# Kernel tuning notes

Measured on AMD Instinct MI355X. Metric: run time of the kernel, lower is better.

The kernel has to match this reference:

```python
import jax, jax.numpy as jnp
import numpy as np

NUM_HEADS = 8
EPS = 1e-6


def setup_inputs() -> dict:
    key = jax.random.key(0)
    k1, k2, k3 = jax.random.split(key, 3)
    B, N, C = 4, 256, 512
    x = jax.random.normal(k1, (B, N, C), dtype=jnp.float32)
    w_qkv = jax.random.normal(k2, (3 * C, C), dtype=jnp.float32) * (C ** -0.5)
    w_proj = jax.random.normal(k3, (C, C), dtype=jnp.float32) * (C ** -0.5)
    b_proj = jnp.zeros((C,), dtype=jnp.float32)
    paramR = jnp.ones((1,), dtype=jnp.float32)
    return {"x": x, "w_qkv": w_qkv, "w_proj": w_proj, "b_proj": b_proj, "paramR": paramR}


def _fourier_attention(x, w_qkv, w_proj, b_proj, paramR):
    B, N, C = x.shape
    H = NUM_HEADS
    Dh = C // H
    # qkv projection (no bias), split into per-head q,k,v: (B,H,N,Dh)
    qkv = jnp.einsum('bnc,kc->bnk', x, w_qkv).reshape(B, N, 3, H, Dh)
    q = qkv[:, :, 0].transpose(0, 2, 1, 3)
    k = qkv[:, :, 1].transpose(0, 2, 1, 3)
    v = qkv[:, :, 2].transpose(0, 2, 1, 3)
    R = paramR[0]
    # Generalized Fourier integral kernel: prod_d sin(R*(q_d - k_d))/(q_d - k_d)
    diff = q[:, :, :, None, :] - k[:, :, None, :, :]  # (B,H,Nq,Nk,Dh)
    near0 = jnp.abs(diff) < 1e-8
    safe = jnp.where(near0, jnp.float32(1.0), diff)
    s = jnp.where(near0, R, jnp.sin(R * safe) / safe)
    score = jnp.prod(s, axis=-1)  # (B,H,Nq,Nk)
    a4 = score ** 4
    attn = a4 / (jnp.sum(a4, axis=-1, keepdims=True) + EPS)  # normalize over keys
    out = jnp.einsum('bhqk,bhkd->bhqd', attn, v)
    out = out.transpose(0, 2, 1, 3).reshape(B, N, C)
    return jnp.einsum('bnc,oc->bno', out, w_proj) + b_proj


def reference(x, w_qkv, w_proj, b_proj, paramR):
    return _fourier_attention(x, w_qkv, w_proj, b_proj, paramR)
```

## Files before the change

kernel.cpp:

```cpp
#include <hip/hip_runtime.h>
#include <math.h>

#define BB 4
#define NN 256
#define CC 512
#define HH 8
#define DH 64

typedef __attribute__((ext_vector_type(8))) short bf16x8;
typedef __attribute__((ext_vector_type(4))) float f32x4;

__device__ inline unsigned short f2bf(float f) {
  unsigned u = __float_as_uint(f);
  u += 0x7FFFu + ((u >> 16) & 1u);
  return (unsigned short)(u >> 16);
}
__device__ inline float bf2f(unsigned short s) {
  return __uint_as_float((unsigned)s << 16);
}

__global__ __launch_bounds__(256) void cvt_hilo(
    const float* __restrict__ in, unsigned short* __restrict__ h,
    unsigned short* __restrict__ l, int n) {
  int i = (blockIdx.x * 256 + threadIdx.x) * 4;
  if (i >= n) return;
  float4 f = *(const float4*)(in + i);
  float fa[4] = {f.x, f.y, f.z, f.w};
  ushort4 hv, lv;
  unsigned short* hp = (unsigned short*)&hv;
  unsigned short* lp = (unsigned short*)&lv;
#pragma unroll
  for (int j = 0; j < 4; j++) {
    unsigned short hb = f2bf(fa[j]);
    hp[j] = hb;
    lp[j] = f2bf(fa[j] - bf2f(hb));
  }
  *(ushort4*)(h + i) = hv;
  *(ushort4*)(l + i) = lv;
}

template <bool BIAS>
__global__ __launch_bounds__(256, 2) void gemm_mfma(
    const unsigned short* __restrict__ Ah, const unsigned short* __restrict__ Al,
    const unsigned short* __restrict__ Bh, const unsigned short* __restrict__ Bl,
    const float* __restrict__ bias, float* __restrict__ C, int M, int N,
    int K) {
  __shared__ unsigned short sAh[128][40], sAl[128][40];
  __shared__ unsigned short sBh[128][40], sBl[128][40];
  const int t = threadIdx.x;
  const int lane = t & 63;
  const int w = t >> 6;
  const int bm = blockIdx.y * 128;
  const int bn = blockIdx.x * 128;
  const int wr = (w >> 1) * 64;
  const int wc = (w & 1) * 64;
  const int quad = lane >> 4;
  const int l16 = lane & 15;

  f32x4 acc[4][4];
#pragma unroll
  for (int i = 0; i < 4; i++)
#pragma unroll
    for (int j = 0; j < 4; j++) {
      acc[i][j][0] = 0.f;
      acc[i][j][1] = 0.f;
      acc[i][j][2] = 0.f;
      acc[i][j][3] = 0.f;
    }

  for (int k0 = 0; k0 < K; k0 += 32) {
    __syncthreads();
#pragma unroll
    for (int s = 0; s < 2; s++) {
      int slot = t + 256 * s;
      int r = slot >> 2;
      int c8 = (slot & 3) * 8;
      *(uint4*)&sAh[r][c8] = *(const uint4*)(Ah + (size_t)(bm + r) * K + k0 + c8);
      *(uint4*)&sAl[r][c8] = *(const uint4*)(Al + (size_t)(bm + r) * K + k0 + c8);
      *(uint4*)&sBh[r][c8] = *(const uint4*)(Bh + (size_t)(bn + r) * K + k0 + c8);
      *(uint4*)&sBl[r][c8] = *(const uint4*)(Bl + (size_t)(bn + r) * K + k0 + c8);
    }
    __syncthreads();

    bf16x8 ah[4], al[4], bh[4], bl[4];
#pragma unroll
    for (int i = 0; i < 4; i++) {
      ah[i] = *(const bf16x8*)&sAh[wr + i * 16 + l16][quad * 8];
      al[i] = *(const bf16x8*)&sAl[wr + i * 16 + l16][quad * 8];
      bh[i] = *(const bf16x8*)&sBh[wc + i * 16 + l16][quad * 8];
      bl[i] = *(const bf16x8*)&sBl[wc + i * 16 + l16][quad * 8];
    }
#pragma unroll
    for (int i = 0; i < 4; i++)
#pragma unroll
      for (int j = 0; j < 4; j++) {
        acc[i][j] = __builtin_amdgcn_mfma_f32_16x16x32_bf16(ah[i], bh[j],
                                                            acc[i][j], 0, 0, 0);
        acc[i][j] = __builtin_amdgcn_mfma_f32_16x16x32_bf16(ah[i], bl[j],
                                                            acc[i][j], 0, 0, 0);
        acc[i][j] = __builtin_amdgcn_mfma_f32_16x16x32_bf16(al[i], bh[j],
                                                            acc[i][j], 0, 0, 0);
      }
  }

#pragma unroll
  for (int i = 0; i < 4; i++)
#pragma unroll
    for (int j = 0; j < 4; j++) {
      int n = bn + wc + j * 16 + l16;
      float bv = BIAS ? bias[n] : 0.f;
#pragma unroll
      for (int r = 0; r < 4; r++) {
        int m = bm + wr + i * 16 + quad * 4 + r;
        C[(size_t)m * N + n] = acc[i][j][r] + bv;
      }
    }
}

__global__ __launch_bounds__(512, 4) void fourier_attn(
    const float* __restrict__ qkv, const float* __restrict__ paramR,
    unsigned short* __restrict__ aoh, unsigned short* __restrict__ aol) {
  __shared__ float Kt[64][68];
  __shared__ float VtT[64][68];
  __shared__ float Qs[16][DH];
  __shared__ float A4[8][64][2];

  const int t = threadIdx.x;
  const int lane = t & 63;
  const int wv = t >> 6;
  const int qc = blockIdx.x;
  const int h = blockIdx.y;
  const int b = blockIdx.z;
  const float R = paramR[0];

  const float* base = qkv + (size_t)b * NN * (3 * CC) + h * DH;

  if (t < 256) {
    int r = t >> 4;
    int c4 = (t & 15) << 2;
    *(float4*)&Qs[r][c4] =
        *(const float4*)(base + (size_t)(qc * 16 + r) * (3 * CC) + c4);
  }

  const int qi0 = wv * 2, qi1 = wv * 2 + 1;
  float Sp[2] = {0.f, 0.f};
  float acc[2] = {0.f, 0.f};

  for (int jt = 0; jt < 4; jt++) {
    __syncthreads();
#pragma unroll
    for (int u0 = 0; u0 < 2; u0++) {
      int u = t + 512 * u0;
      int r = u >> 4;
      int c4 = (u & 15) << 2;
      const float* krow = base + (size_t)(jt * 64 + r) * (3 * CC) + CC;
      *(float4*)&Kt[r][c4] = *(const float4*)(krow + c4);
      const float* vrow = base + (size_t)(jt * 64 + r) * (3 * CC) + 2 * CC;
      float4 vv = *(const float4*)(vrow + c4);
      VtT[c4 + 0][r] = vv.x;
      VtT[c4 + 1][r] = vv.y;
      VtT[c4 + 2][r] = vv.z;
      VtT[c4 + 3][r] = vv.w;
    }
    __syncthreads();

    float nm[2][2] = {{1.f, 1.f}, {1.f, 1.f}};
    float dn[2][2] = {{1.f, 1.f}, {1.f, 1.f}};
#pragma unroll
    for (int d4 = 0; d4 < 16; d4++) {
      const int p = d4 & 1;
      float4 k4 = *(const float4*)&Kt[lane][4 * d4];
      float4 qa = *(const float4*)&Qs[qi0][4 * d4];
      float4 qb = *(const float4*)&Qs[qi1][4 * d4];
      float ka[4] = {k4.x, k4.y, k4.z, k4.w};
      float q0a[4] = {qa.x, qa.y, qa.z, qa.w};
      float q1a[4] = {qb.x, qb.y, qb.z, qb.w};
#pragma unroll
      for (int j = 0; j < 4; j++) {
        float d0 = q0a[j] - ka[j] + 1e-30f;
        float d1 = q1a[j] - ka[j] + 1e-30f;
        nm[0][p] *= __sinf(R * d0);
        dn[0][p] *= d0;
        nm[1][p] *= __sinf(R * d1);
        dn[1][p] *= d1;
      }
    }
#pragma unroll
    for (int q = 0; q < 2; q++) {
      float sc = (nm[q][0] * nm[q][1]) / (dn[q][0] * dn[q][1]);
      float s2 = sc * sc;
      float a4 = s2 * s2;
      Sp[q] += a4;
      A4[wv][lane][q] = a4;
    }

#pragma unroll
    for (int j4 = 0; j4 < 16; j4++) {
      float4 v4 = *(const float4*)&VtT[lane][4 * j4];
      float4 a01 = *(const float4*)&A4[wv][4 * j4 + 0][0];
      float4 a23 = *(const float4*)&A4[wv][4 * j4 + 2][0];
      acc[0] = fmaf(a01.x, v4.x, acc[0]);
      acc[1] = fmaf(a01.y, v4.x, acc[1]);
      acc[0] = fmaf(a01.z, v4.y, acc[0]);
      acc[1] = fmaf(a01.w, v4.y, acc[1]);
      acc[0] = fmaf(a23.x, v4.z, acc[0]);
      acc[1] = fmaf(a23.y, v4.z, acc[1]);
      acc[0] = fmaf(a23.z, v4.w, acc[0]);
      acc[1] = fmaf(a23.w, v4.w, acc[1]);
    }
  }

#pragma unroll
  for (int q = 0; q < 2; q++) {
    float s = Sp[q];
#pragma unroll
    for (int off = 32; off > 0; off >>= 1) s += __shfl_xor(s, off, 64);
    float o = acc[q] / (s + 1e-6f);
    int n = qc * 16 + wv * 2 + q;
    size_t idx = (size_t)(b * NN + n) * CC + h * DH + lane;
    unsigned short oh = f2bf(o);
    aoh[idx] = oh;
    aol[idx] = f2bf(o - bf2f(oh));
  }
}

extern "C" void kernel_launch(void* const* d_in, const int* in_sizes, int n_in,
                              void* d_out, int out_size, void* d_ws,
                              size_t ws_size, hipStream_t stream) {
  const float* x = (const float*)d_in[0];
  const float* w_qkv = (const float*)d_in[1];
  const float* w_proj = (const float*)d_in[2];
  const float* b_proj = (const float*)d_in[3];
  const float* paramR = (const float*)d_in[4];
  float* outp = (float*)d_out;

  const int nX = BB * NN * CC;
  const int nWq = 3 * CC * CC;
  const int nWp = CC * CC;

  unsigned short* xh = (unsigned short*)d_ws;
  unsigned short* xl = xh + nX;
  unsigned short* wqh = xl + nX;
  unsigned short* wql = wqh + nWq;
  unsigned short* wph = wql + nWq;
  unsigned short* wpl = wph + nWp;
  unsigned short* aoh = wpl + nWp;
  unsigned short* aol = aoh + nX;
  float* qkv_ws = (float*)(aol + nX);

  cvt_hilo<<<nX / 1024, 256, 0, stream>>>(x, xh, xl, nX);
  cvt_hilo<<<nWq / 1024, 256, 0, stream>>>(w_qkv, wqh, wql, nWq);
  cvt_hilo<<<nWp / 1024, 256, 0, stream>>>(w_proj, wph, wpl, nWp);

  gemm_mfma<false><<<dim3(3 * CC / 128, BB * NN / 128), 256, 0, stream>>>(
      xh, xl, wqh, wql, nullptr, qkv_ws, BB * NN, 3 * CC, CC);

  fourier_attn<<<dim3(NN / 16, HH, BB), 512, 0, stream>>>(qkv_ws, paramR, aoh,
                                                          aol);

  gemm_mfma<true><<<dim3(CC / 128, BB * NN / 128), 256, 0, stream>>>(
      aoh, aol, wph, wpl, b_proj, outp, BB * NN, CC, CC);
}
```

Measured before the change: 150.4 us.

## Merge conversion kernels, shrink GEMM tiles with register prefetch, swizzle attention V

The three hi/lo bf16 conversion launches become a single launch. The GEMM tile shrinks from 128x128 to 64x64 with a K-step of 64, giving more blocks on the small problem, and the next K-slice is prefetched into registers while MFMAs run. The attention kernel prefetches the next K/V tile into registers and XOR-swizzles the transposed V tile in shared memory to cut bank conflicts. It also swaps __sinf for the raw hardware sin builtin with the argument prescaled by 1/(2π). Smaller GEMM tiles lower per-block reuse, and the raw sin instruction may lose accuracy on large arguments.

```diff
diff --git a/kernel.cpp b/kernel.cpp
--- a/kernel.cpp
+++ b/kernel.cpp
@@ -19,11 +19,23 @@
   return __uint_as_float((unsigned)s << 16);
 }
 
-__global__ __launch_bounds__(256) void cvt_hilo(
-    const float* __restrict__ in, unsigned short* __restrict__ h,
-    unsigned short* __restrict__ l, int n) {
-  int i = (blockIdx.x * 256 + threadIdx.x) * 4;
-  if (i >= n) return;
+__global__ __launch_bounds__(256) void cvt_hilo3(
+    const float* __restrict__ in0, unsigned short* __restrict__ h0,
+    unsigned short* __restrict__ l0, const float* __restrict__ in1,
+    unsigned short* __restrict__ h1, unsigned short* __restrict__ l1,
+    const float* __restrict__ in2, unsigned short* __restrict__ h2,
+    unsigned short* __restrict__ l2) {
+  int b = blockIdx.x;
+  const float* in;
+  unsigned short *h, *l;
+  if (b < 512) {
+    in = in0; h = h0; l = l0;
+  } else if (b < 1280) {
+    in = in1; h = h1; l = l1; b -= 512;
+  } else {
+    in = in2; h = h2; l = l2; b -= 1280;
+  }
+  int i = (b * 256 + threadIdx.x) * 4;
   float4 f = *(const float4*)(in + i);
   float fa[4] = {f.x, f.y, f.z, f.w};
   ushort4 hv, lv;
@@ -45,68 +57,95 @@
     const unsigned short* __restrict__ Bh, const unsigned short* __restrict__ Bl,
     const float* __restrict__ bias, float* __restrict__ C, int M, int N,
     int K) {
-  __shared__ unsigned short sAh[128][40], sAl[128][40];
-  __shared__ unsigned short sBh[128][40], sBl[128][40];
+  __shared__ unsigned short sAh[64][72], sAl[64][72];
+  __shared__ unsigned short sBh[64][72], sBl[64][72];
   const int t = threadIdx.x;
   const int lane = t & 63;
   const int w = t >> 6;
-  const int bm = blockIdx.y * 128;
-  const int bn = blockIdx.x * 128;
-  const int wr = (w >> 1) * 64;
-  const int wc = (w & 1) * 64;
+  const int bm = blockIdx.y * 64;
+  const int bn = blockIdx.x * 64;
+  const int wr = (w >> 1) * 32;
+  const int wc = (w & 1) * 32;
   const int quad = lane >> 4;
   const int l16 = lane & 15;
 
-  f32x4 acc[4][4];
-#pragma unroll
-  for (int i = 0; i < 4; i++)
-#pragma unroll
-    for (int j = 0; j < 4; j++) {
+  const int r0 = t >> 3;
+  const int r1 = r0 + 32;
+  const int c8 = (t & 7) * 8;
+
+  const size_t a0 = (size_t)(bm + r0) * K + c8;
+  const size_t a1 = (size_t)(bm + r1) * K + c8;
+  const size_t b0 = (size_t)(bn + r0) * K + c8;
+  const size_t b1 = (size_t)(bn + r1) * K + c8;
+
+  f32x4 acc[2][2];
+#pragma unroll
+  for (int i = 0; i < 2; i++)
+#pragma unroll
+    for (int j = 0; j < 2; j++) {
       acc[i][j][0] = 0.f;
       acc[i][j][1] = 0.f;
       acc[i][j][2] = 0.f;
       acc[i][j][3] = 0.f;
     }
 
-  for (int k0 = 0; k0 < K; k0 += 32) {
+  uint4 pa0, pa1, pa2, pa3, pb0, pb1, pb2, pb3;
+#define GLOADS(K0)                          \
+  pa0 = *(const uint4*)(Ah + a0 + (K0));    \
+  pa1 = *(const uint4*)(Ah + a1 + (K0));    \
+  pa2 = *(const uint4*)(Al + a0 + (K0));    \
+  pa3 = *(const uint4*)(Al + a1 + (K0));    \
+  pb0 = *(const uint4*)(Bh + b0 + (K0));    \
+  pb1 = *(const uint4*)(Bh + b1 + (K0));    \
+  pb2 = *(const uint4*)(Bl + b0 + (K0));    \
+  pb3 = *(const uint4*)(Bl + b1 + (K0));
+
+  GLOADS(0)
+
+  for (int k0 = 0; k0 < K; k0 += 64) {
     __syncthreads();
-#pragma unroll
-    for (int s = 0; s < 2; s++) {
-      int slot = t + 256 * s;
-      int r = slot >> 2;
-      int c8 = (slot & 3) * 8;
-      *(uint4*)&sAh[r][c8] = *(const uint4*)(Ah + (size_t)(bm + r) * K + k0 + c8);
-      *(uint4*)&sAl[r][c8] = *(const uint4*)(Al + (size_t)(bm + r) * K + k0 + c8);
-      *(uint4*)&sBh[r][c8] = *(const uint4*)(Bh + (size_t)(bn + r) * K + k0 + c8);
-      *(uint4*)&sBl[r][c8] = *(const uint4*)(Bl + (size_t)(bn + r) * K + k0 + c8);
-    }
+    *(uint4*)&sAh[r0][c8] = pa0;
+    *(uint4*)&sAh[r1][c8] = pa1;
+    *(uint4*)&sAl[r0][c8] = pa2;
+    *(uint4*)&sAl[r1][c8] = pa3;
+    *(uint4*)&sBh[r0][c8] = pb0;
+    *(uint4*)&sBh[r1][c8] = pb1;
+    *(uint4*)&sBl[r0][c8] = pb2;
+    *(uint4*)&sBl[r1][c8] = pb3;
     __syncthreads();
-
-    bf16x8 ah[4], al[4], bh[4], bl[4];
-#pragma unroll
-    for (int i = 0; i < 4; i++) {
-      ah[i] = *(const bf16x8*)&sAh[wr + i * 16 + l16][quad * 8];
-      al[i] = *(const bf16x8*)&sAl[wr + i * 16 + l16][quad * 8];
-      bh[i] = *(const bf16x8*)&sBh[wc + i * 16 + l16][quad * 8];
-      bl[i] = *(const bf16x8*)&sBl[wc + i * 16 + l16][quad * 8];
-    }
-#pragma unroll
-    for (int i = 0; i < 4; i++)
-#pragma unroll
-      for (int j = 0; j < 4; j++) {
-        acc[i][j] = __builtin_amdgcn_mfma_f32_16x16x32_bf16(ah[i], bh[j],
-                                                            acc[i][j], 0, 0, 0);
-        acc[i][j] = __builtin_amdgcn_mfma_f32_16x16x32_bf16(ah[i], bl[j],
-                                                            acc[i][j], 0, 0, 0);
-        acc[i][j] = __builtin_amdgcn_mfma_f32_16x16x32_bf16(al[i], bh[j],
-                                                            acc[i][j], 0, 0, 0);
+    if (k0 + 64 < K) {
+      GLOADS(k0 + 64)
+    }
+#pragma unroll
+    for (int kk = 0; kk < 2; kk++) {
+      const int kc = kk * 32 + quad * 8;
+      bf16x8 ah[2], al[2], bh[2], bl[2];
+#pragma unroll
+      for (int i = 0; i < 2; i++) {
+        ah[i] = *(const bf16x8*)&sAh[wr + i * 16 + l16][kc];
+        al[i] = *(const bf16x8*)&sAl[wr + i * 16 + l16][kc];
+        bh[i] = *(const bf16x8*)&sBh[wc + i * 16 + l16][kc];
+        bl[i] = *(const bf16x8*)&sBl[wc + i * 16 + l16][kc];
       }
-  }
-
-#pragma unroll
-  for (int i = 0; i < 4; i++)
-#pragma unroll
-    for (int j = 0; j < 4; j++) {
+#pragma unroll
+      for (int i = 0; i < 2; i++)
+#pragma unroll
+        for (int j = 0; j < 2; j++) {
+          acc[i][j] = __builtin_amdgcn_mfma_f32_16x16x32_bf16(
+              ah[i], bh[j], acc[i][j], 0, 0, 0);
+          acc[i][j] = __builtin_amdgcn_mfma_f32_16x16x32_bf16(
+              ah[i], bl[j], acc[i][j], 0, 0, 0);
+          acc[i][j] = __builtin_amdgcn_mfma_f32_16x16x32_bf16(
+              al[i], bh[j], acc[i][j], 0, 0, 0);
+        }
+    }
+  }
+#undef GLOADS
+
+#pragma unroll
+  for (int i = 0; i < 2; i++)
+#pragma unroll
+    for (int j = 0; j < 2; j++) {
       int n = bn + wc + j * 16 + l16;
       float bv = BIAS ? bias[n] : 0.f;
 #pragma unroll
@@ -132,6 +171,7 @@
   const int h = blockIdx.y;
   const int b = blockIdx.z;
   const float R = paramR[0];
+  const float cR = R * 0.15915494309189535f;
 
   const float* base = qkv + (size_t)b * NN * (3 * CC) + h * DH;
 
@@ -146,6 +186,19 @@
   float Sp[2] = {0.f, 0.f};
   float acc[2] = {0.f, 0.f};
 
+  float4 pk[2], pv[2];
+#define LOADT(JT)                                                   \
+  _Pragma("unroll") for (int u0 = 0; u0 < 2; u0++) {                \
+    int u = t + 512 * u0;                                           \
+    int r_ = u >> 4;                                                \
+    int c4_ = (u & 15) << 2;                                        \
+    const float* row_ = base + (size_t)((JT) * 64 + r_) * (3 * CC); \
+    pk[u0] = *(const float4*)(row_ + CC + c4_);                     \
+    pv[u0] = *(const float4*)(row_ + 2 * CC + c4_);                 \
+  }
+
+  LOADT(0)
+
   for (int jt = 0; jt < 4; jt++) {
     __syncthreads();
 #pragma unroll
@@ -153,16 +206,18 @@
       int u = t + 512 * u0;
       int r = u >> 4;
       int c4 = (u & 15) << 2;
-      const float* krow = base + (size_t)(jt * 64 + r) * (3 * CC) + CC;
-      *(float4*)&Kt[r][c4] = *(const float4*)(krow + c4);
-      const float* vrow = base + (size_t)(jt * 64 + r) * (3 * CC) + 2 * CC;
-      float4 vv = *(const float4*)(vrow + c4);
-      VtT[c4 + 0][r] = vv.x;
-      VtT[c4 + 1][r] = vv.y;
-      VtT[c4 + 2][r] = vv.z;
-      VtT[c4 + 3][r] = vv.w;
+      *(float4*)&Kt[r][c4] = pk[u0];
+      int rs = r ^ c4;
+      float4 vv = pv[u0];
+      VtT[c4 + 0][rs] = vv.x;
+      VtT[c4 + 1][rs] = vv.y;
+      VtT[c4 + 2][rs] = vv.z;
+      VtT[c4 + 3][rs] = vv.w;
     }
     __syncthreads();
+    if (jt < 3) {
+      LOADT(jt + 1)
+    }
 
     float nm[2][2] = {{1.f, 1.f}, {1.f, 1.f}};
     float dn[2][2] = {{1.f, 1.f}, {1.f, 1.f}};
@@ -179,9 +234,9 @@
       for (int j = 0; j < 4; j++) {
         float d0 = q0a[j] - ka[j] + 1e-30f;
         float d1 = q1a[j] - ka[j] + 1e-30f;
-        nm[0][p] *= __sinf(R * d0);
+        nm[0][p] *= __builtin_amdgcn_sinf(cR * d0);
         dn[0][p] *= d0;
-        nm[1][p] *= __sinf(R * d1);
+        nm[1][p] *= __builtin_amdgcn_sinf(cR * d1);
         dn[1][p] *= d1;
       }
     }
@@ -196,7 +251,7 @@
 
 #pragma unroll
     for (int j4 = 0; j4 < 16; j4++) {
-      float4 v4 = *(const float4*)&VtT[lane][4 * j4];
+      float4 v4 = *(const float4*)&VtT[lane][(4 * j4) ^ (lane & 60)];
       float4 a01 = *(const float4*)&A4[wv][4 * j4 + 0][0];
       float4 a23 = *(const float4*)&A4[wv][4 * j4 + 2][0];
       acc[0] = fmaf(a01.x, v4.x, acc[0]);
@@ -209,6 +264,7 @@
       acc[1] = fmaf(a23.w, v4.w, acc[1]);
     }
   }
+#undef LOADT
 
 #pragma unroll
   for (int q = 0; q < 2; q++) {
@@ -248,16 +304,15 @@
   unsigned short* aol = aoh + nX;
   float* qkv_ws = (float*)(aol + nX);
 
-  cvt_hilo<<<nX / 1024, 256, 0, stream>>>(x, xh, xl, nX);
-  cvt_hilo<<<nWq / 1024, 256, 0, stream>>>(w_qkv, wqh, wql, nWq);
-  cvt_hilo<<<nWp / 1024, 256, 0, stream>>>(w_proj, wph, wpl, nWp);
-
-  gemm_mfma<false><<<dim3(3 * CC / 128, BB * NN / 128), 256, 0, stream>>>(
+  cvt_hilo3<<<1536, 256, 0, stream>>>(x, xh, xl, w_qkv, wqh, wql, w_proj, wph,
+                                      wpl);
+
+  gemm_mfma<false><<<dim3(3 * CC / 64, BB * NN / 64), 256, 0, stream>>>(
       xh, xl, wqh, wql, nullptr, qkv_ws, BB * NN, 3 * CC, CC);
 
   fourier_attn<<<dim3(NN / 16, HH, BB), 512, 0, stream>>>(qkv_ws, paramR, aoh,
                                                           aol);
 
-  gemm_mfma<true><<<dim3(CC / 128, BB * NN / 128), 256, 0, stream>>>(
+  gemm_mfma<true><<<dim3(CC / 64, BB * NN / 64), 256, 0, stream>>>(
       aoh, aol, wph, wpl, b_proj, outp, BB * NN, CC, CC);
 }
```

Result: faster. 123.0 us (-18.2%).
